# Optimization experiments

Hardware: AMD Instinct MI355X
Metric: run time of the kernel (lower is better)

The kernel has to match this reference:

```python
import jax, jax.numpy as jnp
import numpy as np

B, S, D, DIM = 8, 4096, 1024, 512  # batch, src nodes, dst nodes, feature dim


def setup_inputs() -> dict:
    key = jax.random.key(0)
    k1, k2, k3, k4, k5 = jax.random.split(key, 5)
    scale = 1.0 / np.sqrt(DIM)
    return {
        "src_val": jax.random.normal(k1, (B, S, DIM), dtype=jnp.float32),
        "src_state": jax.random.normal(k2, (B, S), dtype=jnp.float32),
        "dst_val": jax.random.normal(k3, (B, D, DIM), dtype=jnp.float32),
        "W_route": jax.random.normal(k4, (DIM, DIM), dtype=jnp.float32) * scale,
        "W_val": jax.random.normal(k5, (DIM, DIM), dtype=jnp.float32) * scale,
    }


def reference(src_val, src_state, dst_val, W_route, W_val):
    # Pairwise route logits: bilinear bipartite attention, [B, S, D]
    inv_sqrt_d = 1.0 / jnp.sqrt(jnp.asarray(src_val.shape[-1], src_val.dtype))
    q = jnp.einsum("bsd,de->bse", src_val, W_route)
    logits = jnp.einsum("bse,bke->bsk", q, dst_val) * inv_sqrt_d
    # route compression: softmax over dst nodes (dim=-1)
    routes = jax.nn.softmax(logits, axis=-1)
    # projections
    projected_val = jnp.einsum("bsd,de->bse", src_val, W_val)  # [B, S, DIM]
    projected_state = src_state                                 # identity state proj, [B, S]
    sender_strength = jax.nn.softplus(src_state)                # [B, S]
    # weighted routing + accumulation
    weighted_routes = routes * sender_strength[..., None]       # [B, S, D]
    delta_state = jnp.einsum("bsk,bs->bk", weighted_routes, projected_state)   # [B, D]
    delta_val = jnp.einsum("bsk,bsd->bkd", weighted_routes, projected_val)     # [B, D, DIM]
    return delta_state, delta_val
```

## Files before the change

### kernel.cpp

```cpp
#include <hip/hip_runtime.h>
#include <hip/hip_fp16.h>

#define B_   8
#define S_   4096
#define DD_  1024
#define DIM_ 512
#define SCALE 0.044194173824159216f
#define PPN  ((size_t)B_ * DD_ * DIM_)

typedef __bf16 bf16x8 __attribute__((ext_vector_type(8)));
typedef float  floatx4 __attribute__((ext_vector_type(4)));

__device__ inline unsigned short f2bf(float f) {
    union { float f; unsigned int u; } v; v.f = f;
    unsigned int r = v.u + 0x7fffu + ((v.u >> 16) & 1u);
    return (unsigned short)(r >> 16);
}
__device__ inline float bf2f(unsigned short h) {
    union { unsigned int u; float f; } v; v.u = ((unsigned int)h) << 16;
    return v.f;
}
__device__ inline uint4 cvt8(const float* __restrict__ g) {
    float4 f0 = *(const float4*)g;
    float4 f1 = *(const float4*)(g + 4);
    unsigned short tmp[8] = {f2bf(f0.x), f2bf(f0.y), f2bf(f0.z), f2bf(f0.w),
                             f2bf(f1.x), f2bf(f1.y), f2bf(f1.z), f2bf(f1.w)};
    return *(const uint4*)tmp;
}
__device__ inline void async16(unsigned short* lds, const unsigned short* g) {
    __builtin_amdgcn_global_load_lds(
        (const __attribute__((address_space(1))) void*)g,
        (__attribute__((address_space(3))) void*)lds, 16, 0, 0);
}

template <int N> __device__ inline void vwait() {
    if constexpr (N == 0)      asm volatile("s_waitcnt vmcnt(0)" ::: "memory");
    else if constexpr (N == 4) asm volatile("s_waitcnt vmcnt(4)" ::: "memory");
    else if constexpr (N == 6) asm volatile("s_waitcnt vmcnt(6)" ::: "memory");
    else                       asm volatile("s_waitcnt vmcnt(8)" ::: "memory");
}
#define SBAR   __builtin_amdgcn_s_barrier()
#define SCHED0 __builtin_amdgcn_sched_barrier(0)

__device__ inline void mainloop256(unsigned short* As, unsigned short* Bs,
                                   const unsigned short* __restrict__ Ap, size_t lda,
                                   const unsigned short* __restrict__ Bp, size_t ldb,
                                   int nk, floatx4 (&acc)[8][4]) {
    const int t = threadIdx.x, lane = t & 63, w = t >> 6;
    const int wm = w >> 2, wn = w & 3;
    const int fr = lane & 15;
    const int swz  = (((lane >> 4) ^ ((fr >> 1) & 3)) << 3);
    const int csrc = (((t & 3) ^ ((t >> 3) & 3)) << 3);

    const unsigned short* gA = Ap + (size_t)(t >> 2) * lda + csrc;
    const unsigned short* gB = Bp + (size_t)(t >> 2) * ldb + csrc;
    unsigned short* ldsA = As + w * 512;
    unsigned short* ldsB = Bs + w * 512;

    auto stgA = [&](int buf, int kt, int kh) {
        const unsigned short* g = gA + (size_t)kt * 64 + kh * 32;
        async16(ldsA + buf * 16384 + kh * 8192,        g);
        async16(ldsA + buf * 16384 + kh * 8192 + 4096, g + (size_t)128 * lda);
    };
    auto stgB = [&](int buf, int kt, int kh) {
        const unsigned short* g = gB + (size_t)kt * 64 + kh * 32;
        async16(ldsB + buf * 16384 + kh * 8192,        g);
        async16(ldsB + buf * 16384 + kh * 8192 + 4096, g + (size_t)128 * ldb);
    };

    stgA(0, 0, 0); stgB(0, 0, 0); stgA(0, 0, 1); stgB(0, 0, 1);
    stgA(1, 1, 0); stgB(1, 1, 0);
    vwait<8>();
    SCHED0;
    SBAR;

    const int arow = wm * 128 + fr, brow = wn * 64 + fr;
    bf16x8 a0[4], b0[4], a1[4], a2[4], b2[4], a3[4];
#pragma unroll
    for (int i = 0; i < 4; ++i) a0[i] = *(const bf16x8*)&As[(arow + i * 16) * 32 + swz];
#pragma unroll
    for (int j = 0; j < 4; ++j) b0[j] = *(const bf16x8*)&Bs[(brow + j * 16) * 32 + swz];

    for (int kt = 0; kt < nk; ++kt) {
        const int cur = kt & 1, base = cur * 16384;
        const bool sA = kt + 1 < nk, sB = kt + 2 < nk;
        if (sA) stgA(cur ^ 1, kt + 1, 1);
        SCHED0;
        __builtin_amdgcn_s_setprio(1);
#pragma unroll
        for (int i = 0; i < 4; ++i)
            a1[i] = *(const bf16x8*)&As[base + (arow + 64 + i * 16) * 32 + swz];
#pragma unroll
        for (int i = 0; i < 4; ++i)
#pragma unroll
            for (int j = 0; j < 4; ++j)
                acc[i][j] = __builtin_amdgcn_mfma_f32_16x16x32_bf16(a0[i], b0[j], acc[i][j], 0, 0, 0);
        __builtin_amdgcn_s_setprio(0);
        if (sA) vwait<6>(); else vwait<0>();
        SBAR;
        if (sA) stgB(cur ^ 1, kt + 1, 1);
        SCHED0;
        __builtin_amdgcn_s_setprio(1);
#pragma unroll
        for (int i = 0; i < 4; ++i)
            a2[i] = *(const bf16x8*)&As[base + 8192 + (arow + i * 16) * 32 + swz];
#pragma unroll
        for (int j = 0; j < 4; ++j)
            b2[j] = *(const bf16x8*)&Bs[base + 8192 + (brow + j * 16) * 32 + swz];
#pragma unroll
        for (int i = 0; i < 4; ++i)
#pragma unroll
            for (int j = 0; j < 4; ++j)
                acc[4 + i][j] = __builtin_amdgcn_mfma_f32_16x16x32_bf16(a1[i], b0[j], acc[4 + i][j], 0, 0, 0);
        __builtin_amdgcn_s_setprio(0);
        SBAR;
        if (sB) stgA(cur, kt + 2, 0);
        SCHED0;
        __builtin_amdgcn_s_setprio(1);
#pragma unroll
        for (int i = 0; i < 4; ++i)
            a3[i] = *(const bf16x8*)&As[base + 8192 + (arow + 64 + i * 16) * 32 + swz];
#pragma unroll
        for (int i = 0; i < 4; ++i)
#pragma unroll
            for (int j = 0; j < 4; ++j)
                acc[i][j] = __builtin_amdgcn_mfma_f32_16x16x32_bf16(a2[i], b2[j], acc[i][j], 0, 0, 0);
        __builtin_amdgcn_s_setprio(0);
        if (sA) { if (sB) vwait<6>(); else vwait<4>(); }
        SBAR;
        if (sB) stgB(cur, kt + 2, 0);
        SCHED0;
        __builtin_amdgcn_s_setprio(1);
        if (sA) {
            const int nb = (cur ^ 1) * 16384;
#pragma unroll
            for (int i = 0; i < 4; ++i)
                a0[i] = *(const bf16x8*)&As[nb + (arow + i * 16) * 32 + swz];
#pragma unroll
            for (int j = 0; j < 4; ++j)
                b0[j] = *(const bf16x8*)&Bs[nb + (brow + j * 16) * 32 + swz];
        }
#pragma unroll
        for (int i = 0; i < 4; ++i)
#pragma unroll
            for (int j = 0; j < 4; ++j)
                acc[4 + i][j] = __builtin_amdgcn_mfma_f32_16x16x32_bf16(a3[i], b2[j], acc[4 + i][j], 0, 0, 0);
        __builtin_amdgcn_s_setprio(0);
        SBAR;
    }
}

#define ACC_INIT8                                           \
    floatx4 acc[8][4];                                      \
    _Pragma("unroll") for (int i = 0; i < 8; ++i)           \
        _Pragma("unroll") for (int j = 0; j < 4; ++j)       \
            acc[i][j] = (floatx4){0.f, 0.f, 0.f, 0.f};

template <int AF32, int BF32>
__device__ inline void mainloop(unsigned short* As, unsigned short* Bs,
                                const void* Ap, size_t lda,
                                const void* Bp, size_t ldb,
                                int kIters, floatx4 (&acc)[4][4]) {
    const int t = threadIdx.x, lane = t & 63, wave = t >> 6;
    const int rA = t >> 2;
    const int cA = ((t & 3) ^ ((t >> 3) & 3)) * 8;
    const int mrow = (wave >> 1) * 64, ncol = (wave & 1) * 64;
    const int fr = lane & 15, fk = (lane >> 4) * 8;
    const int swz = (((fk >> 3) ^ ((fr >> 1) & 3)) << 3);

    const unsigned short* gA16 = nullptr; const float* gA32 = nullptr;
    const unsigned short* gB16 = nullptr; const float* gB32 = nullptr;
    if (AF32) gA32 = (const float*)Ap + (size_t)rA * lda + cA;
    else      gA16 = (const unsigned short*)Ap + (size_t)rA * lda + cA;
    if (BF32) gB32 = (const float*)Bp + (size_t)rA * ldb + cA;
    else      gB16 = (const unsigned short*)Bp + (size_t)rA * ldb + cA;

    unsigned short* ldsA = As + wave * 512;
    unsigned short* ldsB = Bs + wave * 512;

    auto stage = [&](int buf) {
        const int o = buf * 4096;
        if (AF32) {
            *(uint4*)&As[o + t * 8]        = cvt8(gA32);
            *(uint4*)&As[o + 2048 + t * 8] = cvt8(gA32 + 64 * lda);
            gA32 += 32;
        } else {
            async16(ldsA + o,        gA16);
            async16(ldsA + o + 2048, gA16 + 64 * lda);
            gA16 += 32;
        }
        if (BF32) {
            *(uint4*)&Bs[o + t * 8]        = cvt8(gB32);
            *(uint4*)&Bs[o + 2048 + t * 8] = cvt8(gB32 + 64 * ldb);
            gB32 += 32;
        } else {
            async16(ldsB + o,        gB16);
            async16(ldsB + o + 2048, gB16 + 64 * ldb);
            gB16 += 32;
        }
    };

    stage(0);
    __syncthreads();
    for (int kt = 0; kt < kIters; ++kt) {
        if (kt + 1 < kIters) stage((kt + 1) & 1);
        const int cur = (kt & 1) * 4096;
        bf16x8 af[4], bfr[4];
#pragma unroll
        for (int i = 0; i < 4; ++i)
            af[i] = *(const bf16x8*)&As[cur + (mrow + i * 16 + fr) * 32 + swz];
#pragma unroll
        for (int j = 0; j < 4; ++j)
            bfr[j] = *(const bf16x8*)&Bs[cur + (ncol + j * 16 + fr) * 32 + swz];
#pragma unroll
        for (int i = 0; i < 4; ++i)
#pragma unroll
            for (int j = 0; j < 4; ++j)
                acc[i][j] = __builtin_amdgcn_mfma_f32_16x16x32_bf16(af[i], bfr[j],
                                                                    acc[i][j], 0, 0, 0);
        __syncthreads();
    }
}

#define EPILOGUE_COORDS                                     \
    const int lane = threadIdx.x & 63, wave = threadIdx.x >> 6; \
    const int mrow = (wave >> 1) * 64, ncol = (wave & 1) * 64;  \
    const int col = lane & 15, q = lane >> 4;

#define ACC_INIT                                            \
    floatx4 acc[4][4];                                      \
    _Pragma("unroll") for (int i = 0; i < 4; ++i)           \
        _Pragma("unroll") for (int j = 0; j < 4; ++j)       \
            acc[i][j] = (floatx4){0.f, 0.f, 0.f, 0.f};

__global__ __launch_bounds__(256) void k_prep(const float* __restrict__ src,
                                              unsigned short* __restrict__ srcb) {
    const size_t idx = ((size_t)blockIdx.x * 256 + threadIdx.x) * 8;
    *(uint4*)&srcb[idx] = cvt8(src + idx);
}

__global__ __launch_bounds__(256) void k_dstWr(const float* __restrict__ dst,
                                               const float* __restrict__ Wr,
                                               unsigned short* __restrict__ DW) {
    __shared__ unsigned short As[2 * 128 * 32];
    __shared__ unsigned short Bs[2 * 128 * 32];
    const int n0 = blockIdx.x * 128, m0 = blockIdx.y * 128;
    ACC_INIT
    mainloop<1, 1>(As, Bs, dst + (size_t)m0 * DIM_, DIM_,
                   Wr + (size_t)n0 * DIM_, DIM_, DIM_ / 32, acc);
    EPILOGUE_COORDS
#pragma unroll
    for (int i = 0; i < 4; ++i)
#pragma unroll
        for (int j = 0; j < 4; ++j)
#pragma unroll
            for (int r = 0; r < 4; ++r)
                DW[(size_t)(m0 + mrow + i * 16 + q * 4 + r) * DIM_ +
                   n0 + ncol + j * 16 + col] = f2bf(acc[i][j][r] * SCALE);
}

__global__ __launch_bounds__(512, 2) void k_logitsT(const unsigned short* __restrict__ DW,
                                                    const unsigned short* __restrict__ srcb,
                                                    unsigned short* __restrict__ LTb,
                                                    float* __restrict__ Lpart) {
    __shared__ __align__(16) unsigned short As[32768];
    __shared__ __align__(16) unsigned short Bs[32768];
    const int n = blockIdx.x;
    const int b = n & 7;
    const int rem = n >> 3;
    const int xs = rem >> 2;
    const int yd = rem & 3;
    const int n0 = xs * 256, m0 = yd * 256;
    ACC_INIT8
    mainloop256(As, Bs,
                DW + (size_t)b * DD_ * DIM_ + (size_t)m0 * DIM_, DIM_,
                srcb + (size_t)b * S_ * DIM_ + (size_t)n0 * DIM_, DIM_,
                DIM_ / 64, acc);
    const int t = threadIdx.x, lane = t & 63, w = t >> 6;
    const int wm = w >> 2, wn = w & 3;
    const int c16 = lane & 15, q = lane >> 4;
    const int row0 = m0 + wm * 128, col0 = n0 + wn * 64;
    unsigned short* LT = LTb + (size_t)b * DD_ * S_;
    float psum[4] = {0.f, 0.f, 0.f, 0.f};
#pragma unroll
    for (int i = 0; i < 8; ++i)
#pragma unroll
        for (int j = 0; j < 4; ++j)
#pragma unroll
            for (int r = 0; r < 4; ++r) {
                float e = __expf(acc[i][j][r]);
                LT[(size_t)(row0 + i * 16 + q * 4 + r) * S_ +
                   col0 + j * 16 + c16] = f2bf(e);
                psum[j] += e;
            }
    float* csum = (float*)As;
    const int slice = wm * 4 + q;
#pragma unroll
    for (int j = 0; j < 4; ++j)
        csum[slice * 256 + wn * 64 + j * 16 + c16] = psum[j];
    __syncthreads();
    if (t < 256) {
        float v = 0.f;
#pragma unroll
        for (int k = 0; k < 8; ++k) v += csum[k * 256 + t];
        Lpart[((size_t)b * 4 + yd) * S_ + n0 + t] = v;
    }
}

__global__ __launch_bounds__(256) void k_finalize(const float* __restrict__ state,
                                                  const float* __restrict__ Lpart,
                                                  float* __restrict__ scale,
                                                  float* __restrict__ w) {
    const int i = blockIdx.x * 256 + threadIdx.x;
    const int b = i >> 12, s = i & (S_ - 1);
    float d = 0.f;
#pragma unroll
    for (int k = 0; k < 4; ++k) d += Lpart[((size_t)b * 4 + k) * S_ + s];
    const float st = state[i];
    const float sp = (st > 15.f) ? st : log1pf(__expf(st));
    const float sc = sp / d;
    scale[i] = sc;
    w[i] = sc * st;
}

__global__ __launch_bounds__(256) void k_mid(const unsigned short* __restrict__ LTb,
                                             const float* __restrict__ w,
                                             const unsigned short* __restrict__ srcb,
                                             const float* __restrict__ scale,
                                             unsigned short* __restrict__ srcST,
                                             float* __restrict__ out) {
    __shared__ unsigned short Ts[64 * 65];
    const int bx = blockIdx.x;
    const int t = threadIdx.x;
    if (bx < 2048) {
        const int b = bx >> 8;
        const int dd = (bx & 255) * 4 + (t >> 6);
        const int lane = t & 63;
        const unsigned short* row = LTb + (size_t)b * DD_ * S_ + (size_t)dd * S_;
        const float* wp = w + (size_t)b * S_;
        float acc = 0.f;
#pragma unroll
        for (int it = 0; it < S_ / 512; ++it) {
            const int s = it * 512 + lane * 8;
            uint4 v = *(const uint4*)(row + s);
            const unsigned short* e = (const unsigned short*)&v;
            float4 w0 = *(const float4*)(wp + s);
            float4 w1 = *(const float4*)(wp + s + 4);
            acc += bf2f(e[0]) * w0.x + bf2f(e[1]) * w0.y +
                   bf2f(e[2]) * w0.z + bf2f(e[3]) * w0.w +
                   bf2f(e[4]) * w1.x + bf2f(e[5]) * w1.y +
                   bf2f(e[6]) * w1.z + bf2f(e[7]) * w1.w;
        }
#pragma unroll
        for (int off = 32; off; off >>= 1) acc += __shfl_down(acc, off);
        if (lane == 0) out[(size_t)b * DD_ + dd] = acc;
        return;
    }
    const int i2 = bx - 2048;
    const int s0 = (i2 & 63) * 64, d0 = ((i2 >> 6) & 7) * 64, b = i2 >> 9;
    {
        const int r = t >> 2, c0 = (t & 3) * 16;
        const unsigned short* g =
            srcb + (size_t)b * S_ * DIM_ + (size_t)(s0 + r) * DIM_ + d0 + c0;
        uint4 v0 = *(const uint4*)g;
        uint4 v1 = *(const uint4*)(g + 8);
        const unsigned short* e0 = (const unsigned short*)&v0;
        const unsigned short* e1 = (const unsigned short*)&v1;
        const float sc = scale[(size_t)b * S_ + s0 + r];
#pragma unroll
        for (int i = 0; i < 8; ++i) {
            Ts[r * 65 + c0 + i]     = f2bf(bf2f(e0[i]) * sc);
            Ts[r * 65 + c0 + 8 + i] = f2bf(bf2f(e1[i]) * sc);
        }
    }
    __syncthreads();
    {
        const int rr = t >> 2, c0 = (t & 3) * 16;
        unsigned short tmp[16];
#pragma unroll
        for (int j = 0; j < 16; ++j) tmp[j] = Ts[(c0 + j) * 65 + rr];
        unsigned short* o =
            srcST + (size_t)b * DIM_ * S_ + (size_t)(d0 + rr) * S_ + s0 + c0;
        *(uint4*)o = *(const uint4*)tmp;
        *(uint4*)(o + 8) = *(const uint4*)(tmp + 8);
    }
}

__global__ __launch_bounds__(512, 2) void k_dU(const unsigned short* __restrict__ LTb,
                                               const unsigned short* __restrict__ srcST,
                                               __half* __restrict__ Pp) {
    __shared__ __align__(16) unsigned short As[32768];
    __shared__ __align__(16) unsigned short Bs[32768];
    const int n = blockIdx.x;
    const int qn = n >> 3;
    const int tile = qn & 7, zhi = qn >> 3;
    const int z = (n & 7) + 8 * zhi;
    const int b = z >> 2, ks = z & 3;
    const int xe = tile >> 2;
    const int yd = tile & 3;
    const int n0 = xe * 256, m0 = yd * 256;
    ACC_INIT8
    mainloop256(As, Bs,
                LTb + (size_t)b * DD_ * S_ + (size_t)m0 * S_ + ks * 1024, S_,
                srcST + (size_t)b * DIM_ * S_ + (size_t)n0 * S_ + ks * 1024, S_,
                1024 / 64, acc);
    const int t = threadIdx.x, lane = t & 63, w = t >> 6;
    const int wm = w >> 2, wn = w & 3;
    const int c16 = lane & 15, q = lane >> 4;
    const int row0 = m0 + wm * 128, col0 = n0 + wn * 64;
    __half* O = Pp + (size_t)ks * PPN + (size_t)b * DD_ * DIM_;
#pragma unroll
    for (int i = 0; i < 8; ++i)
#pragma unroll
        for (int j = 0; j < 4; ++j)
#pragma unroll
            for (int r = 0; r < 4; ++r)
                O[(size_t)(row0 + i * 16 + q * 4 + r) * DIM_ +
                  col0 + j * 16 + c16] = __float2half(acc[i][j][r]);
}

__global__ __launch_bounds__(256) void k_dvalW2(const __half* __restrict__ Pp,
                                                const float* __restrict__ Wv,
                                                float* __restrict__ d_val) {
    __shared__ unsigned short As[2 * 128 * 32];
    __shared__ unsigned short Bs[2 * 128 * 32];
    const int n0 = blockIdx.x * 128, m0 = blockIdx.y * 128;
    const int t = threadIdx.x;
    const int rA = t >> 2, cA = ((t & 3) ^ ((t >> 3) & 3)) * 8;
    const __half* gA = Pp + (size_t)(m0 + rA) * DIM_ + cA;
    const int d0 = (t >> 4) * 2;
    const int ecol = t & 15;

    ACC_INIT
    auto stageA8 = [&](unsigned short* dst, const __half* g) {
        float o[8] = {0.f, 0.f, 0.f, 0.f, 0.f, 0.f, 0.f, 0.f};
#pragma unroll
        for (int ksl = 0; ksl < 4; ++ksl) {
            uint4 v = *(const uint4*)(g + (size_t)ksl * PPN);
            const __half* h = (const __half*)&v;
#pragma unroll
            for (int j = 0; j < 8; ++j) o[j] += __half2float(h[j]);
        }
        unsigned short tmp[8];
#pragma unroll
        for (int j = 0; j < 8; ++j) tmp[j] = f2bf(o[j]);
        *(uint4*)dst = *(const uint4*)tmp;
    };
    auto stage = [&](int buf, int kt) {
        const int o = buf * 4096;
        stageA8(&As[o + t * 8],        gA + kt * 32);
        stageA8(&As[o + 2048 + t * 8], gA + kt * 32 + (size_t)64 * DIM_);
        const float* wv = Wv + (size_t)(kt * 32 + d0) * DIM_ + n0 + ecol;
#pragma unroll
        for (int i = 0; i < 8; ++i) {
            float v0 = wv[16 * i];
            float v1 = wv[16 * i + DIM_];
            unsigned int pk = (unsigned int)f2bf(v0) | ((unsigned int)f2bf(v1) << 16);
            const int e = ecol + 16 * i;
            const int phys = e * 32 + (((d0 >> 3) ^ ((e >> 1) & 3)) << 3) + (d0 & 7);
            *(unsigned int*)&Bs[o + phys] = pk;
        }
    };

    stage(0, 0);
    __syncthreads();
    const int lane = t & 63, wave = t >> 6;
    const int mrow = (wave >> 1) * 64, ncol = (wave & 1) * 64;
    const int fr = lane & 15, fk = (lane >> 4) * 8;
    const int swz = (((fk >> 3) ^ ((fr >> 1) & 3)) << 3);
    for (int kt = 0; kt < DIM_ / 32; ++kt) {
        if (kt + 1 < DIM_ / 32) stage((kt + 1) & 1, kt + 1);
        const int cur = (kt & 1) * 4096;
        bf16x8 af[4], bfr[4];
#pragma unroll
        for (int i = 0; i < 4; ++i)
            af[i] = *(const bf16x8*)&As[cur + (mrow + i * 16 + fr) * 32 + swz];
#pragma unroll
        for (int j = 0; j < 4; ++j)
            bfr[j] = *(const bf16x8*)&Bs[cur + (ncol + j * 16 + fr) * 32 + swz];
#pragma unroll
        for (int i = 0; i < 4; ++i)
#pragma unroll
            for (int j = 0; j < 4; ++j)
                acc[i][j] = __builtin_amdgcn_mfma_f32_16x16x32_bf16(af[i], bfr[j],
                                                                    acc[i][j], 0, 0, 0);
        __syncthreads();
    }
    const int col = lane & 15, q = lane >> 4;
#pragma unroll
    for (int i = 0; i < 4; ++i)
#pragma unroll
        for (int j = 0; j < 4; ++j)
#pragma unroll
            for (int r = 0; r < 4; ++r)
                d_val[(size_t)(m0 + mrow + i * 16 + q * 4 + r) * DIM_ +
                      n0 + ncol + j * 16 + col] = acc[i][j][r];
}

extern "C" void kernel_launch(void* const* d_in, const int* in_sizes, int n_in,
                              void* d_out, int out_size, void* d_ws, size_t ws_size,
                              hipStream_t stream) {
    const float* src   = (const float*)d_in[0];
    const float* state = (const float*)d_in[1];
    const float* dst   = (const float*)d_in[2];
    const float* Wr    = (const float*)d_in[3];
    const float* Wv    = (const float*)d_in[4];

    unsigned short* srcb = (unsigned short*)d_ws;
    __half* Pp = (__half*)d_ws;
    unsigned short* LT = srcb + (size_t)B_ * S_ * DIM_;
    unsigned short* C = LT + (size_t)B_ * DD_ * S_;
    unsigned short* DW = C;
    float* Lpart = (float*)(DW + (size_t)B_ * DD_ * DIM_);
    unsigned short* srcST = C;

    float* d_state = (float*)d_out;
    float* d_val   = (float*)d_out + B_ * DD_;
    float* scale   = d_val;
    float* w       = d_val + (size_t)B_ * S_;

    k_prep<<<dim3(8192), 256, 0, stream>>>(src, srcb);
    k_dstWr<<<dim3(DIM_ / 128, (B_ * DD_) / 128), 256, 0, stream>>>(dst, Wr, DW);
    k_logitsT<<<dim3(512), 512, 0, stream>>>(DW, srcb, LT, Lpart);
    k_finalize<<<dim3((B_ * S_) / 256), 256, 0, stream>>>(state, Lpart, scale, w);
    k_mid<<<dim3(2048 + 4096), 256, 0, stream>>>(LT, w, srcb, scale, srcST, d_state);
    k_dU<<<dim3(256), 512, 0, stream>>>(LT, srcST, Pp);
    k_dvalW2<<<dim3(DIM_ / 128, (B_ * DD_) / 128), 256, 0, stream>>>(Pp, Wv, d_val);
}
```

Measured before the change: 288.8 us.

## Load B operand directly from global into registers, dropping its LDS staging

The B tile in the 256x256 GEMM mainloop is no longer staged through shared memory. Each wave now gathers its own B fragments straight from global memory into registers, one k-half ahead, and the vmcnt waits are retuned to the new count of outstanding loads. This removes the LDS writes and reads for B, halves LDS use per block, and may allow higher occupancy. The cost is that each of the two wm wave rows loads the same B data separately, so global/L2 traffic for B doubles, and the register loads are exposed to global latency with less lookahead.

```diff
diff --git a/kernel.cpp b/kernel.cpp
--- a/kernel.cpp
+++ b/kernel.cpp
@@ -34,15 +34,17 @@
 }
 
 template <int N> __device__ inline void vwait() {
-    if constexpr (N == 0)      asm volatile("s_waitcnt vmcnt(0)" ::: "memory");
-    else if constexpr (N == 4) asm volatile("s_waitcnt vmcnt(4)" ::: "memory");
-    else if constexpr (N == 6) asm volatile("s_waitcnt vmcnt(6)" ::: "memory");
-    else                       asm volatile("s_waitcnt vmcnt(8)" ::: "memory");
+    if constexpr (N == 0)       asm volatile("s_waitcnt vmcnt(0)"  ::: "memory");
+    else if constexpr (N == 4)  asm volatile("s_waitcnt vmcnt(4)"  ::: "memory");
+    else if constexpr (N == 6)  asm volatile("s_waitcnt vmcnt(6)"  ::: "memory");
+    else if constexpr (N == 8)  asm volatile("s_waitcnt vmcnt(8)"  ::: "memory");
+    else if constexpr (N == 10) asm volatile("s_waitcnt vmcnt(10)" ::: "memory");
+    else                        asm volatile("s_waitcnt vmcnt(12)" ::: "memory");
 }
 #define SBAR   __builtin_amdgcn_s_barrier()
 #define SCHED0 __builtin_amdgcn_sched_barrier(0)
 
-__device__ inline void mainloop256(unsigned short* As, unsigned short* Bs,
+__device__ inline void mainloop256(unsigned short* As,
                                    const unsigned short* __restrict__ Ap, size_t lda,
                                    const unsigned short* __restrict__ Bp, size_t ldb,
                                    int nk, floatx4 (&acc)[8][4]) {
@@ -53,33 +55,33 @@
     const int csrc = (((t & 3) ^ ((t >> 3) & 3)) << 3);
 
     const unsigned short* gA = Ap + (size_t)(t >> 2) * lda + csrc;
-    const unsigned short* gB = Bp + (size_t)(t >> 2) * ldb + csrc;
+    const unsigned short* pB = Bp + (size_t)(wn * 64 + fr) * ldb + (lane >> 4) * 8;
     unsigned short* ldsA = As + w * 512;
-    unsigned short* ldsB = Bs + w * 512;
 
     auto stgA = [&](int buf, int kt, int kh) {
         const unsigned short* g = gA + (size_t)kt * 64 + kh * 32;
         async16(ldsA + buf * 16384 + kh * 8192,        g);
         async16(ldsA + buf * 16384 + kh * 8192 + 4096, g + (size_t)128 * lda);
     };
-    auto stgB = [&](int buf, int kt, int kh) {
-        const unsigned short* g = gB + (size_t)kt * 64 + kh * 32;
-        async16(ldsB + buf * 16384 + kh * 8192,        g);
-        async16(ldsB + buf * 16384 + kh * 8192 + 4096, g + (size_t)128 * ldb);
+    auto gatherB = [&](bf16x8 (&dst)[4], int kt, int kh) {
+#pragma unroll
+        for (int n = 0; n < 4; ++n) {
+            uint4 v = *(const uint4*)(pB + (size_t)n * 16 * ldb + kt * 64 + kh * 32);
+            dst[n] = *(const bf16x8*)&v;
+        }
     };
 
-    stgA(0, 0, 0); stgB(0, 0, 0); stgA(0, 0, 1); stgB(0, 0, 1);
-    stgA(1, 1, 0); stgB(1, 1, 0);
+    stgA(0, 0, 0); stgA(0, 0, 1); stgA(1, 1, 0);
+    bf16x8 bA[4], bB[4];
+    gatherB(bA, 0, 0);
     vwait<8>();
     SCHED0;
     SBAR;
 
-    const int arow = wm * 128 + fr, brow = wn * 64 + fr;
-    bf16x8 a0[4], b0[4], a1[4], a2[4], b2[4], a3[4];
+    const int arow = wm * 128 + fr;
+    bf16x8 a0[4], a1[4], a2[4], a3[4];
 #pragma unroll
     for (int i = 0; i < 4; ++i) a0[i] = *(const bf16x8*)&As[(arow + i * 16) * 32 + swz];
-#pragma unroll
-    for (int j = 0; j < 4; ++j) b0[j] = *(const bf16x8*)&Bs[(brow + j * 16) * 32 + swz];
 
     for (int kt = 0; kt < nk; ++kt) {
         const int cur = kt & 1, base = cur * 16384;
@@ -94,24 +96,21 @@
         for (int i = 0; i < 4; ++i)
 #pragma unroll
             for (int j = 0; j < 4; ++j)
-                acc[i][j] = __builtin_amdgcn_mfma_f32_16x16x32_bf16(a0[i], b0[j], acc[i][j], 0, 0, 0);
+                acc[i][j] = __builtin_amdgcn_mfma_f32_16x16x32_bf16(a0[i], bA[j], acc[i][j], 0, 0, 0);
         __builtin_amdgcn_s_setprio(0);
-        if (sA) vwait<6>(); else vwait<0>();
+        if (sA) { if (kt == 0) vwait<8>(); else vwait<12>(); } else vwait<0>();
         SBAR;
-        if (sA) stgB(cur ^ 1, kt + 1, 1);
+        gatherB(bB, kt, 1);
         SCHED0;
         __builtin_amdgcn_s_setprio(1);
 #pragma unroll
         for (int i = 0; i < 4; ++i)
             a2[i] = *(const bf16x8*)&As[base + 8192 + (arow + i * 16) * 32 + swz];
 #pragma unroll
-        for (int j = 0; j < 4; ++j)
-            b2[j] = *(const bf16x8*)&Bs[base + 8192 + (brow + j * 16) * 32 + swz];
-#pragma unroll
         for (int i = 0; i < 4; ++i)
 #pragma unroll
             for (int j = 0; j < 4; ++j)
-                acc[4 + i][j] = __builtin_amdgcn_mfma_f32_16x16x32_bf16(a1[i], b0[j], acc[4 + i][j], 0, 0, 0);
+                acc[4 + i][j] = __builtin_amdgcn_mfma_f32_16x16x32_bf16(a1[i], bA[j], acc[4 + i][j], 0, 0, 0);
         __builtin_amdgcn_s_setprio(0);
         SBAR;
         if (sB) stgA(cur, kt + 2, 0);
@@ -124,11 +123,11 @@
         for (int i = 0; i < 4; ++i)
 #pragma unroll
             for (int j = 0; j < 4; ++j)
-                acc[i][j] = __builtin_amdgcn_mfma_f32_16x16x32_bf16(a2[i], b2[j], acc[i][j], 0, 0, 0);
+                acc[i][j] = __builtin_amdgcn_mfma_f32_16x16x32_bf16(a2[i], bB[j], acc[i][j], 0, 0, 0);
         __builtin_amdgcn_s_setprio(0);
-        if (sA) { if (sB) vwait<6>(); else vwait<4>(); }
+        if (sA) { if (sB) vwait<12>(); else vwait<10>(); }
         SBAR;
-        if (sB) stgB(cur, kt + 2, 0);
+        if (sA) gatherB(bA, kt + 1, 0);
         SCHED0;
         __builtin_amdgcn_s_setprio(1);
         if (sA) {
@@ -136,15 +135,12 @@
 #pragma unroll
             for (int i = 0; i < 4; ++i)
                 a0[i] = *(const bf16x8*)&As[nb + (arow + i * 16) * 32 + swz];
+        }
+#pragma unroll
+        for (int i = 0; i < 4; ++i)
 #pragma unroll
             for (int j = 0; j < 4; ++j)
-                b0[j] = *(const bf16x8*)&Bs[nb + (brow + j * 16) * 32 + swz];
-        }
-#pragma unroll
-        for (int i = 0; i < 4; ++i)
-#pragma unroll
-            for (int j = 0; j < 4; ++j)
-                acc[4 + i][j] = __builtin_amdgcn_mfma_f32_16x16x32_bf16(a3[i], b2[j], acc[4 + i][j], 0, 0, 0);
+                acc[4 + i][j] = __builtin_amdgcn_mfma_f32_16x16x32_bf16(a3[i], bB[j], acc[4 + i][j], 0, 0, 0);
         __builtin_amdgcn_s_setprio(0);
         SBAR;
     }
@@ -264,7 +260,6 @@
                                                     unsigned short* __restrict__ LTb,
                                                     float* __restrict__ Lpart) {
     __shared__ __align__(16) unsigned short As[32768];
-    __shared__ __align__(16) unsigned short Bs[32768];
     const int n = blockIdx.x;
     const int b = n & 7;
     const int rem = n >> 3;
@@ -272,7 +267,7 @@
     const int yd = rem & 3;
     const int n0 = xs * 256, m0 = yd * 256;
     ACC_INIT8
-    mainloop256(As, Bs,
+    mainloop256(As,
                 DW + (size_t)b * DD_ * DIM_ + (size_t)m0 * DIM_, DIM_,
                 srcb + (size_t)b * S_ * DIM_ + (size_t)n0 * DIM_, DIM_,
                 DIM_ / 64, acc);
@@ -390,7 +385,6 @@
                                                const unsigned short* __restrict__ srcST,
                                                __half* __restrict__ Pp) {
     __shared__ __align__(16) unsigned short As[32768];
-    __shared__ __align__(16) unsigned short Bs[32768];
     const int n = blockIdx.x;
     const int qn = n >> 3;
     const int tile = qn & 7, zhi = qn >> 3;
@@ -400,7 +394,7 @@
     const int yd = tile & 3;
     const int n0 = xe * 256, m0 = yd * 256;
     ACC_INIT8
-    mainloop256(As, Bs,
+    mainloop256(As,
                 LTb + (size_t)b * DD_ * S_ + (size_t)m0 * S_ + ks * 1024, S_,
                 srcST + (size_t)b * DIM_ * S_ + (size_t)n0 * S_ + ks * 1024, S_,
                 1024 / 64, acc);
```

Measured after the change: 315.4 us. 9.2% more time.
